# Kernel tuning notes

Measured on AMD Instinct MI355X. Metric: run time of the kernel, lower is better.

## Reference

```python
import jax, jax.numpy as jnp
import numpy as np

EMBED = 512
HEADS = 1
HEAD_DIM = EMBED // HEADS  # 512 (heads must be 1 for the original torch code to run)
N, S = 4, 4096


def setup_inputs() -> dict:
    key = jax.random.key(0)
    ks = jax.random.split(key, 9)
    scale = 1.0 / np.sqrt(EMBED)
    return {
        "values": jax.random.normal(ks[0], (N, 1, S, EMBED), dtype=jnp.float32),
        "keys": jax.random.normal(ks[1], (N, 1, S, EMBED), dtype=jnp.float32),
        "query": jax.random.normal(ks[2], (N, 1, S, EMBED), dtype=jnp.float32),
        "mask": jax.random.randint(ks[3], (N, 1, S, S), 0, 2, dtype=jnp.int32),
        "Wv": jax.random.normal(ks[4], (EMBED, EMBED), dtype=jnp.float32) * scale,
        "Wk": jax.random.normal(ks[5], (EMBED, EMBED), dtype=jnp.float32) * scale,
        "Wq": jax.random.normal(ks[6], (EMBED, EMBED), dtype=jnp.float32) * scale,
        "Wo": jax.random.normal(ks[7], (EMBED, EMBED), dtype=jnp.float32) * scale,
        "bo": jnp.zeros((EMBED,), dtype=jnp.float32),
    }


def reference(values, keys, query, mask, Wv, Wk, Wq, Wo, bo):
    n = query.shape[0]
    q_len = query.shape[2]
    # reshape(N, -1, heads, head_dim); inputs are [N, 1, S, E] -> [N, S, H, Dh]
    v = values.reshape(n, -1, HEADS, HEAD_DIM)
    k = keys.reshape(n, -1, HEADS, HEAD_DIM)
    q = query.reshape(n, -1, HEADS, HEAD_DIM)
    # per-module linear projections (nn.Linear: y = x @ W.T)
    v = jnp.einsum('nlhd,ed->nlhe', v, Wv)
    k = jnp.einsum('nlhd,ed->nlhe', k, Wk)
    q = jnp.einsum('nqhd,ed->nqhe', q, Wq)
    # full [N, H, Q, K] score matrix, as in the original
    energy = jnp.einsum('nqhd,nkhd->nhqk', q, k)
    energy = jnp.where(mask == 0, jnp.float32(-1e20), energy)
    attn = jax.nn.softmax(energy / np.sqrt(HEAD_DIM), axis=3)
    out = jnp.einsum('nhql,nlhd->nqhd', attn, v).reshape(n, q_len, HEADS * HEAD_DIM)
    return out @ Wo.T + bo
```

## Files before the change

### kernel.cpp

```cpp
#include <hip/hip_runtime.h>

typedef __bf16 bf16x8 __attribute__((ext_vector_type(8)));
typedef __bf16 bf16x4 __attribute__((ext_vector_type(4)));
typedef float f32x4 __attribute__((ext_vector_type(4)));
typedef float f32x16 __attribute__((ext_vector_type(16)));

#define MFMA16(a, b, c) __builtin_amdgcn_mfma_f32_16x16x32_bf16((a), (b), (c), 0, 0, 0)
#define MFMA32(a, b, c) __builtin_amdgcn_mfma_f32_32x32x16_bf16((a), (b), (c), 0, 0, 0)

static constexpr int SEQ = 4096;
static constexpr int DIM = 512;

typedef __attribute__((address_space(3))) void lds_void;
typedef __attribute__((address_space(1))) const void gbl_void;

__device__ __forceinline__ void glds16(const void* g, void* l) {
    __builtin_amdgcn_global_load_lds((gbl_void*)g, (lds_void*)l, 16, 0, 0);
}

__device__ __forceinline__ bf16x8 cvt8f(const float* __restrict__ p) {
    float4 f0 = *(const float4*)p;
    float4 f1 = *(const float4*)(p + 4);
    bf16x8 v;
    v[0] = (__bf16)f0.x; v[1] = (__bf16)f0.y; v[2] = (__bf16)f0.z; v[3] = (__bf16)f0.w;
    v[4] = (__bf16)f1.x; v[5] = (__bf16)f1.y; v[6] = (__bf16)f1.z; v[7] = (__bf16)f1.w;
    return v;
}

__global__ __launch_bounds__(256)
void cvt_f32_bf16(const float* __restrict__ in, __bf16* __restrict__ out) {
    const size_t i = ((size_t)blockIdx.x * 256 + threadIdx.x) * 8;
    *(bf16x8*)(out + i) = cvt8f(in + i);
}

__global__ __launch_bounds__(256)
void convert_w(const float* __restrict__ wq, const float* __restrict__ wk,
               const float* __restrict__ wv, const float* __restrict__ wo,
               __bf16* __restrict__ out)
{
    const int z = blockIdx.y;
    const float* src = (z == 0) ? wq : (z == 1) ? wk : (z == 2) ? wv : wo;
    __bf16* dst = out + (size_t)z * DIM * DIM;
    const int i = (blockIdx.x * 256 + threadIdx.x) * 8;
    *(bf16x8*)(dst + i) = cvt8f(src + i);
}

template <bool TRANS>
__global__ __launch_bounds__(256, 3)
void gemm_bf16(const __bf16* __restrict__ Ap, const __bf16* __restrict__ Bp,
               __bf16* __restrict__ Cp)
{
    __shared__ __align__(16) char smem[128 * 132 * 2];
    __bf16* As = (__bf16*)smem;
    __bf16* Bs = (__bf16*)(smem + 16384);

    const int tid  = threadIdx.x;
    const int wave = tid >> 6;
    const int lane = tid & 63;
    const int quad = lane >> 4;
    const int l16  = lane & 15;
    const int m0 = blockIdx.x * 128;
    const int n0 = blockIdx.y * 128;
    const int wm = (wave >> 1) * 64;
    const int wn = (wave & 1) * 64;

    f32x4 acc[4][4] = {};

    for (int k0 = 0; k0 < DIM; k0 += 64) {
        #pragma unroll
        for (int i = 0; i < 4; i++) {
            const int j = wave * 4 + i;
            const int c = j * 64 + lane;
            const int row = c >> 3, c8 = c & 7;
            glds16(Ap + (size_t)(m0 + row) * DIM + k0 + c8 * 8, &As[j * 512]);
            glds16(Bp + (size_t)(n0 + row) * DIM + k0 + c8 * 8, &Bs[j * 512]);
        }
        __syncthreads();
        #pragma unroll
        for (int kk = 0; kk < 2; kk++) {
            bf16x8 af[4], bg[4];
            #pragma unroll
            for (int mt = 0; mt < 4; mt++)
                af[mt] = *(const bf16x8*)&As[(wm + mt * 16 + l16) * 64 + kk * 32 + quad * 8];
            #pragma unroll
            for (int nt = 0; nt < 4; nt++)
                bg[nt] = *(const bf16x8*)&Bs[(wn + nt * 16 + l16) * 64 + kk * 32 + quad * 8];
            #pragma unroll
            for (int mt = 0; mt < 4; mt++)
                #pragma unroll
                for (int nt = 0; nt < 4; nt++)
                    acc[mt][nt] = MFMA16(af[mt], bg[nt], acc[mt][nt]);
        }
        __syncthreads();
    }

    if (!TRANS) {
        #pragma unroll
        for (int mt = 0; mt < 4; mt++)
            #pragma unroll
            for (int nt = 0; nt < 4; nt++)
                #pragma unroll
                for (int r = 0; r < 4; r++)
                    Cp[(size_t)(m0 + wm + mt * 16 + quad * 4 + r) * DIM
                       + n0 + wn + nt * 16 + l16] = (__bf16)acc[mt][nt][r];
    } else {
        __bf16* Tt = (__bf16*)smem;
        #pragma unroll
        for (int mt = 0; mt < 4; mt++)
            #pragma unroll
            for (int nt = 0; nt < 4; nt++)
                #pragma unroll
                for (int r = 0; r < 4; r++)
                    Tt[(wm + mt * 16 + quad * 4 + r) * 132 + wn + nt * 16 + l16]
                        = (__bf16)acc[mt][nt][r];
        __syncthreads();
        const int nb  = m0 >> 12;
        const int s0m = m0 & 4095;
        const int d   = tid >> 1;
        const int sh  = (tid & 1) * 64;
        __bf16* dst = Cp + (size_t)nb * DIM * SEQ + (size_t)(n0 + d) * SEQ + s0m + sh;
        #pragma unroll
        for (int i = 0; i < 8; i++) {
            bf16x8 vv;
            #pragma unroll
            for (int e = 0; e < 8; e++) vv[e] = Tt[(sh + i * 8 + e) * 132 + d];
            *(bf16x8*)(dst + i * 8) = vv;
        }
    }
}

__global__ __launch_bounds__(256, 3)
void gemm_out(const __bf16* __restrict__ Ap, const __bf16* __restrict__ Bp,
              float* __restrict__ Cp, const float* __restrict__ bias)
{
    __shared__ __align__(16) __bf16 As[128 * 64];
    __shared__ __align__(16) __bf16 Bs[128 * 64];
    const int tid  = threadIdx.x;
    const int wave = tid >> 6;
    const int lane = tid & 63;
    const int quad = lane >> 4;
    const int l16  = lane & 15;
    const int m0 = blockIdx.x * 128;
    const int n0 = blockIdx.y * 128;
    const int wm = (wave >> 1) * 64;
    const int wn = (wave & 1) * 64;

    f32x4 acc[4][4] = {};

    for (int k0 = 0; k0 < DIM; k0 += 64) {
        #pragma unroll
        for (int i = 0; i < 4; i++) {
            const int j = wave * 4 + i;
            const int c = j * 64 + lane;
            const int row = c >> 3, c8 = c & 7;
            glds16(Ap + (size_t)(m0 + row) * DIM + k0 + c8 * 8, &As[j * 512]);
            glds16(Bp + (size_t)(n0 + row) * DIM + k0 + c8 * 8, &Bs[j * 512]);
        }
        __syncthreads();
        #pragma unroll
        for (int kk = 0; kk < 2; kk++) {
            bf16x8 af[4], bg[4];
            #pragma unroll
            for (int mt = 0; mt < 4; mt++)
                af[mt] = *(const bf16x8*)&As[(wm + mt * 16 + l16) * 64 + kk * 32 + quad * 8];
            #pragma unroll
            for (int nt = 0; nt < 4; nt++)
                bg[nt] = *(const bf16x8*)&Bs[(wn + nt * 16 + l16) * 64 + kk * 32 + quad * 8];
            #pragma unroll
            for (int mt = 0; mt < 4; mt++)
                #pragma unroll
                for (int nt = 0; nt < 4; nt++)
                    acc[mt][nt] = MFMA16(af[mt], bg[nt], acc[mt][nt]);
        }
        __syncthreads();
    }
    #pragma unroll
    for (int mt = 0; mt < 4; mt++)
        #pragma unroll
        for (int nt = 0; nt < 4; nt++)
            #pragma unroll
            for (int r = 0; r < 4; r++) {
                const int col = n0 + wn + nt * 16 + l16;
                Cp[(size_t)(m0 + wm + mt * 16 + quad * 4 + r) * DIM + col]
                    = acc[mt][nt][r] + bias[col];
            }
}

__global__ __launch_bounds__(512, 2)
void flash_attn(__bf16* __restrict__ Qp, const __bf16* __restrict__ Kp,
                const __bf16* __restrict__ Vt, const int* __restrict__ mask)
{
    constexpr float SCALE = 0.044194173824159216f;

    __shared__ __bf16 Qs[64 * 512];
    __shared__ __bf16 KV[256 * 64];
    __shared__ __bf16 P[64 * 256];
    __shared__ unsigned Wb[8 * 66];
    __shared__ float pmax[8 * 66];
    __shared__ float psum[8 * 66];

    const int bid  = blockIdx.x;
    const int n    = bid & 3;
    const int q0   = (bid >> 2) * 64;
    const int tid  = threadIdx.x;
    const int w    = tid >> 6;
    const int lane = tid & 63;
    const int l32  = lane & 31;
    const int half = lane >> 5;
    const int r8   = lane >> 3;
    const int c8   = lane & 7;
    const int gc   = c8 ^ r8;

    const __bf16* Qb = Qp + (size_t)n * SEQ * DIM;
    const __bf16* Kb = Kp + (size_t)n * SEQ * DIM;
    const __bf16* Vb = Vt + (size_t)n * DIM * SEQ;
    const int*    Mb = mask + (size_t)n * SEQ * SEQ;
    __bf16*       AO = Qp + (size_t)n * SEQ * DIM;

    #pragma unroll
    for (int i = 0; i < 8; i++) {
        const int row = i * 8 + w;
        const int cs  = (lane & 56) | ((lane & 7) ^ (row & 7));
        glds16(Qb + (size_t)(q0 + row) * DIM + cs * 8, &Qs[row * 512]);
    }

    float m0 = -__builtin_inff(), m1 = -__builtin_inff();
    float l0 = 0.f, l1 = 0.f;
    f32x16 o00 = {}, o01 = {}, o10 = {}, o11 = {};

    const int mq = tid >> 3;
    const int wd = tid & 7;

    #pragma unroll 1
    for (int j = 0; j < 16; j++) {
        const int k0 = j * 256;

        int4 mk[8];
        {
            const int* mp = Mb + (size_t)(q0 + mq) * SEQ + k0 + wd * 32;
            #pragma unroll
            for (int c = 0; c < 8; c++) mk[c] = *(const int4*)(mp + c * 4);
        }

        f32x16 s0 = {}, s1 = {};
        #pragma unroll 1
        for (int dc = 0; dc < 8; dc++) {
            #pragma unroll
            for (int i = 0; i < 4; i++) {
                const int R = (i * 8 + w) * 8 + r8;
                glds16(Kb + (size_t)(k0 + R) * DIM + dc * 64 + gc * 8,
                       &KV[(i * 8 + w) * 512]);
            }
            __syncthreads();
            #pragma unroll
            for (int ks = 0; ks < 4; ks++) {
                const int row = 32 * w + l32;
                const int ca  = (2 * ks + half) ^ (row & 7);
                bf16x8 a = *(const bf16x8*)&KV[row * 64 + ca * 8];
                const int cq = dc * 8 + 2 * ks + half;
                const int pq = (cq & 56) | ((cq & 7) ^ (l32 & 7));
                bf16x8 b0 = *(const bf16x8*)&Qs[l32 * 512 + pq * 8];
                bf16x8 b1 = *(const bf16x8*)&Qs[(32 + l32) * 512 + pq * 8];
                s0 = MFMA32(a, b0, s0);
                s1 = MFMA32(a, b1, s1);
            }
            __syncthreads();
        }

        {
            unsigned wv = 0;
            #pragma unroll
            for (int c = 0; c < 8; c++) {
                wv |= (unsigned)(mk[c].x & 1) << (c * 4);
                wv |= (unsigned)(mk[c].y & 1) << (c * 4 + 1);
                wv |= (unsigned)(mk[c].z & 1) << (c * 4 + 2);
                wv |= (unsigned)(mk[c].w & 1) << (c * 4 + 3);
            }
            Wb[wd * 66 + mq] = wv;
        }
        {
            float mx0 = s0[0], mx1 = s1[0];
            #pragma unroll
            for (int r = 1; r < 16; r++) { mx0 = fmaxf(mx0, s0[r]); mx1 = fmaxf(mx1, s1[r]); }
            mx0 = fmaxf(mx0, __shfl_xor(mx0, 32));
            mx1 = fmaxf(mx1, __shfl_xor(mx1, 32));
            if (half == 0) pmax[w * 66 + l32]      = mx0;
            else           pmax[w * 66 + 32 + l32] = mx1;
        }
        __syncthreads();

        float mp0 = pmax[l32], mp1 = pmax[32 + l32];
        #pragma unroll
        for (int w2 = 1; w2 < 8; w2++) {
            mp0 = fmaxf(mp0, pmax[w2 * 66 + l32]);
            mp1 = fmaxf(mp1, pmax[w2 * 66 + 32 + l32]);
        }
        const float mn0 = fmaxf(m0, mp0 * SCALE);
        const float mn1 = fmaxf(m1, mp1 * SCALE);
        const float a0 = __expf(m0 - mn0);
        const float a1 = __expf(m1 - mn1);
        m0 = mn0; m1 = mn1;
        #pragma unroll
        for (int r = 0; r < 16; r++) {
            o00[r] *= a0; o10[r] *= a0;
            o01[r] *= a1; o11[r] *= a1;
        }

        float ls0 = 0.f, ls1 = 0.f;
        {
            const unsigned wm0 = Wb[w * 66 + l32];
            const unsigned wm1 = Wb[w * 66 + 32 + l32];
            #pragma unroll
            for (int g = 0; g < 4; g++) {
                bf16x4 pv0, pv1;
                #pragma unroll
                for (int r4 = 0; r4 < 4; r4++) {
                    const int r = g * 4 + r4;
                    const int bit = g * 8 + half * 4 + r4;
                    float p0 = __expf(s0[r] * SCALE - mn0);
                    float p1 = __expf(s1[r] * SCALE - mn1);
                    p0 = ((wm0 >> bit) & 1u) ? p0 : 0.f;
                    p1 = ((wm1 >> bit) & 1u) ? p1 : 0.f;
                    ls0 += p0; ls1 += p1;
                    pv0[r4] = (__bf16)p0;
                    pv1[r4] = (__bf16)p1;
                }
                const int c  = 4 * w + g;
                const int cp = (c & 24) | ((c & 7) ^ (l32 & 7));
                *(bf16x4*)&P[l32 * 256 + cp * 8 + 4 * half]        = pv0;
                *(bf16x4*)&P[(32 + l32) * 256 + cp * 8 + 4 * half] = pv1;
            }
            ls0 += __shfl_xor(ls0, 32);
            ls1 += __shfl_xor(ls1, 32);
            if (half == 0) psum[w * 66 + l32]      = ls0;
            else           psum[w * 66 + 32 + l32] = ls1;
        }
        __syncthreads();

        {
            float ss0 = 0.f, ss1 = 0.f;
            #pragma unroll
            for (int w2 = 0; w2 < 8; w2++) {
                ss0 += psum[w2 * 66 + l32];
                ss1 += psum[w2 * 66 + 32 + l32];
            }
            l0 = l0 * a0 + ss0;
            l1 = l1 * a1 + ss1;
        }

        #pragma unroll 1
        for (int h = 0; h < 2; h++) {
            #pragma unroll 1
            for (int kc2 = 0; kc2 < 4; kc2++) {
                #pragma unroll
                for (int i = 0; i < 4; i++) {
                    const int R = (i * 8 + w) * 8 + r8;
                    glds16(Vb + (size_t)(h * 256 + R) * SEQ + k0 + kc2 * 64 + gc * 8,
                           &KV[(i * 8 + w) * 512]);
                }
                __syncthreads();
                #pragma unroll
                for (int ks = 0; ks < 4; ks++) {
                    const int row = 32 * w + l32;
                    const int ca  = (2 * ks + half) ^ (row & 7);
                    bf16x8 a = *(const bf16x8*)&KV[row * 64 + ca * 8];
                    const int ck = kc2 * 8 + 2 * ks + half;
                    const int cp = (ck & 24) | ((ck & 7) ^ (l32 & 7));
                    bf16x8 b0 = *(const bf16x8*)&P[l32 * 256 + cp * 8];
                    bf16x8 b1 = *(const bf16x8*)&P[(32 + l32) * 256 + cp * 8];
                    if (h == 0) { o00 = MFMA32(a, b0, o00); o01 = MFMA32(a, b1, o01); }
                    else        { o10 = MFMA32(a, b0, o10); o11 = MFMA32(a, b1, o11); }
                }
                __syncthreads();
            }
        }
    }

    const float li0 = 1.f / l0, li1 = 1.f / l1;
    __bf16* ao0 = AO + (size_t)(q0 + l32) * DIM;
    __bf16* ao1 = AO + (size_t)(q0 + 32 + l32) * DIM;
    #pragma unroll
    for (int h = 0; h < 2; h++) {
        #pragma unroll
        for (int g = 0; g < 4; g++) {
            bf16x4 v00, v01;
            #pragma unroll
            for (int r4 = 0; r4 < 4; r4++) {
                const int r = g * 4 + r4;
                v00[r4] = (__bf16)((h ? o10[r] : o00[r]) * li0);
                v01[r4] = (__bf16)((h ? o11[r] : o01[r]) * li1);
            }
            const int d = h * 256 + 32 * w + g * 8 + 4 * half;
            *(bf16x4*)&ao0[d] = v00;
            *(bf16x4*)&ao1[d] = v01;
        }
    }
}

extern "C" void kernel_launch(void* const* d_in, const int* in_sizes, int n_in,
                              void* d_out, int out_size, void* d_ws, size_t ws_size,
                              hipStream_t stream)
{
    const float* values = (const float*)d_in[0];
    const float* keys   = (const float*)d_in[1];
    const float* query  = (const float*)d_in[2];
    const int*   mask   = (const int*)d_in[3];
    const float* Wv = (const float*)d_in[4];
    const float* Wk = (const float*)d_in[5];
    const float* Wq = (const float*)d_in[6];
    const float* Wo = (const float*)d_in[7];
    const float* bo = (const float*)d_in[8];
    float* out = (float*)d_out;

    char* ws = (char*)d_ws;
    __bf16* Qp  = (__bf16*)(ws);
    __bf16* Kp  = (__bf16*)(ws + (16u << 20));
    __bf16* Vt  = (__bf16*)(ws + (32u << 20));
    __bf16* Abf = (__bf16*)(ws + (48u << 20));
    __bf16* wbf = (__bf16*)(ws + (64u << 20));

    const int M = 4 * SEQ;
    const dim3 gg(M / 128, DIM / 128);

    convert_w<<<dim3(128, 4), 256, 0, stream>>>(Wq, Wk, Wv, Wo, wbf);

    cvt_f32_bf16<<<4096, 256, 0, stream>>>(query, Abf);
    gemm_bf16<false><<<gg, 256, 0, stream>>>(Abf, wbf + 0 * DIM * DIM, Qp);

    cvt_f32_bf16<<<4096, 256, 0, stream>>>(keys, Abf);
    gemm_bf16<false><<<gg, 256, 0, stream>>>(Abf, wbf + 1 * DIM * DIM, Kp);

    cvt_f32_bf16<<<4096, 256, 0, stream>>>(values, Abf);
    gemm_bf16<true><<<gg, 256, 0, stream>>>(Abf, wbf + 2 * DIM * DIM, Vt);

    flash_attn<<<256, 512, 0, stream>>>(Qp, Kp, Vt, mask);

    gemm_out<<<gg, 256, 0, stream>>>(Qp , wbf + 3 * DIM * DIM, out, bo);
}
```

Measured before the change: 808.9 us.

## Double-buffer K/V/Q staging in flash attention and load mask per-thread directly

Replaces the single K/V LDS buffer and resident full Q tile with a two-slot ring buffer. Each slot holds a K or V chunk plus the matching 64-column Q slice, and the next chunk is prefetched while MFMAs run on the current one, which halves the barriers per chunk. Mask values are loaded straight into the register layout of the score fragment, removing the bit-packed LDS mask exchange. MFMA phases are wrapped in s_setprio. Occupancy is lowered to one 512-thread block per CU and Q is reloaded from global memory for every key block.

```diff
diff --git a/kernel.cpp b/kernel.cpp
--- a/kernel.cpp
+++ b/kernel.cpp
@@ -186,16 +186,16 @@
             }
 }
 
-__global__ __launch_bounds__(512, 2)
+#define MKC(v, r4) ((r4) == 0 ? (v).x : (r4) == 1 ? (v).y : (r4) == 2 ? (v).z : (v).w)
+
+__global__ __launch_bounds__(512, 1)
 void flash_attn(__bf16* __restrict__ Qp, const __bf16* __restrict__ Kp,
                 const __bf16* __restrict__ Vt, const int* __restrict__ mask)
 {
     constexpr float SCALE = 0.044194173824159216f;
 
-    __shared__ __bf16 Qs[64 * 512];
-    __shared__ __bf16 KV[256 * 64];
+    __shared__ __bf16 KQ[2][20480];
     __shared__ __bf16 P[64 * 256];
-    __shared__ unsigned Wb[8 * 66];
     __shared__ float pmax[8 * 66];
     __shared__ float psum[8 * 66];
 
@@ -217,86 +217,92 @@
     const int*    Mb = mask + (size_t)n * SEQ * SEQ;
     __bf16*       AO = Qp + (size_t)n * SEQ * DIM;
 
-    #pragma unroll
-    for (int i = 0; i < 8; i++) {
-        const int row = i * 8 + w;
-        const int cs  = (lane & 56) | ((lane & 7) ^ (row & 7));
-        glds16(Qb + (size_t)(q0 + row) * DIM + cs * 8, &Qs[row * 512]);
-    }
+    auto stageK = [&](int slot, int k0, int dc) {
+        #pragma unroll
+        for (int i = 0; i < 4; i++) {
+            const int R = (i * 8 + w) * 8 + r8;
+            glds16(Kb + (size_t)(k0 + R) * DIM + dc * 64 + gc * 8,
+                   &KQ[slot][(i * 8 + w) * 512]);
+        }
+    };
+    auto stageV = [&](int slot, int k0, int vc) {
+        const int h = vc >> 2, kc2 = vc & 3;
+        #pragma unroll
+        for (int i = 0; i < 4; i++) {
+            const int R = (i * 8 + w) * 8 + r8;
+            glds16(Vb + (size_t)(h * 256 + R) * SEQ + k0 + kc2 * 64 + gc * 8,
+                   &KQ[slot][(i * 8 + w) * 512]);
+        }
+    };
+    auto stageQ = [&](int slot, int dc) {
+        glds16(Qb + (size_t)(q0 + w * 8 + r8) * DIM + dc * 64 + gc * 8,
+               &KQ[slot][16384 + w * 512]);
+    };
 
     float m0 = -__builtin_inff(), m1 = -__builtin_inff();
     float l0 = 0.f, l1 = 0.f;
     f32x16 o00 = {}, o01 = {}, o10 = {}, o11 = {};
 
-    const int mq = tid >> 3;
-    const int wd = tid & 7;
+    stageK(0, 0, 0);
+    stageQ(0, 0);
+    __syncthreads();
+    int cur = 0;
 
     #pragma unroll 1
     for (int j = 0; j < 16; j++) {
         const int k0 = j * 256;
 
-        int4 mk[8];
+        int4 mk0[4], mk1[4];
         {
-            const int* mp = Mb + (size_t)(q0 + mq) * SEQ + k0 + wd * 32;
-            #pragma unroll
-            for (int c = 0; c < 8; c++) mk[c] = *(const int4*)(mp + c * 4);
+            const int* mp0 = Mb + (size_t)(q0 + l32) * SEQ + k0 + 32 * w + 4 * half;
+            const int* mp1 = mp0 + (size_t)32 * SEQ;
+            #pragma unroll
+            for (int g = 0; g < 4; g++) {
+                mk0[g] = *(const int4*)(mp0 + 8 * g);
+                mk1[g] = *(const int4*)(mp1 + 8 * g);
+            }
         }
 
         f32x16 s0 = {}, s1 = {};
         #pragma unroll 1
         for (int dc = 0; dc < 8; dc++) {
-            #pragma unroll
-            for (int i = 0; i < 4; i++) {
-                const int R = (i * 8 + w) * 8 + r8;
-                glds16(Kb + (size_t)(k0 + R) * DIM + dc * 64 + gc * 8,
-                       &KV[(i * 8 + w) * 512]);
-            }
-            __syncthreads();
+            const int nxt = cur ^ 1;
+            if (dc < 7) { stageK(nxt, k0, dc + 1); stageQ(nxt, dc + 1); }
+            else        { stageV(nxt, k0, 0); }
+            const __bf16* Kc = KQ[cur];
+            const __bf16* Qc = KQ[cur] + 16384;
+            __builtin_amdgcn_s_setprio(1);
             #pragma unroll
             for (int ks = 0; ks < 4; ks++) {
-                const int row = 32 * w + l32;
-                const int ca  = (2 * ks + half) ^ (row & 7);
-                bf16x8 a = *(const bf16x8*)&KV[row * 64 + ca * 8];
-                const int cq = dc * 8 + 2 * ks + half;
-                const int pq = (cq & 56) | ((cq & 7) ^ (l32 & 7));
-                bf16x8 b0 = *(const bf16x8*)&Qs[l32 * 512 + pq * 8];
-                bf16x8 b1 = *(const bf16x8*)&Qs[(32 + l32) * 512 + pq * 8];
+                const int ch = (2 * ks + half) ^ (l32 & 7);
+                bf16x8 a  = *(const bf16x8*)&Kc[(32 * w + l32) * 64 + ch * 8];
+                bf16x8 b0 = *(const bf16x8*)&Qc[l32 * 64 + ch * 8];
+                bf16x8 b1 = *(const bf16x8*)&Qc[(32 + l32) * 64 + ch * 8];
                 s0 = MFMA32(a, b0, s0);
                 s1 = MFMA32(a, b1, s1);
             }
+            __builtin_amdgcn_s_setprio(0);
+            if (dc == 7) {
+                float mx0 = s0[0], mx1 = s1[0];
+                #pragma unroll
+                for (int r = 1; r < 16; r++) { mx0 = fmaxf(mx0, s0[r]); mx1 = fmaxf(mx1, s1[r]); }
+                mx0 = fmaxf(mx0, __shfl_xor(mx0, 32));
+                mx1 = fmaxf(mx1, __shfl_xor(mx1, 32));
+                if (half == 0) pmax[w * 66 + l32]      = mx0;
+                else           pmax[w * 66 + 32 + l32] = mx1;
+            }
             __syncthreads();
-        }
-
-        {
-            unsigned wv = 0;
-            #pragma unroll
-            for (int c = 0; c < 8; c++) {
-                wv |= (unsigned)(mk[c].x & 1) << (c * 4);
-                wv |= (unsigned)(mk[c].y & 1) << (c * 4 + 1);
-                wv |= (unsigned)(mk[c].z & 1) << (c * 4 + 2);
-                wv |= (unsigned)(mk[c].w & 1) << (c * 4 + 3);
-            }
-            Wb[wd * 66 + mq] = wv;
-        }
-        {
-            float mx0 = s0[0], mx1 = s1[0];
-            #pragma unroll
-            for (int r = 1; r < 16; r++) { mx0 = fmaxf(mx0, s0[r]); mx1 = fmaxf(mx1, s1[r]); }
-            mx0 = fmaxf(mx0, __shfl_xor(mx0, 32));
-            mx1 = fmaxf(mx1, __shfl_xor(mx1, 32));
-            if (half == 0) pmax[w * 66 + l32]      = mx0;
-            else           pmax[w * 66 + 32 + l32] = mx1;
-        }
-        __syncthreads();
-
-        float mp0 = pmax[l32], mp1 = pmax[32 + l32];
+            cur = nxt;
+        }
+
+        float mp0v = pmax[l32], mp1v = pmax[32 + l32];
         #pragma unroll
         for (int w2 = 1; w2 < 8; w2++) {
-            mp0 = fmaxf(mp0, pmax[w2 * 66 + l32]);
-            mp1 = fmaxf(mp1, pmax[w2 * 66 + 32 + l32]);
-        }
-        const float mn0 = fmaxf(m0, mp0 * SCALE);
-        const float mn1 = fmaxf(m1, mp1 * SCALE);
+            mp0v = fmaxf(mp0v, pmax[w2 * 66 + l32]);
+            mp1v = fmaxf(mp1v, pmax[w2 * 66 + 32 + l32]);
+        }
+        const float mn0 = fmaxf(m0, mp0v * SCALE);
+        const float mn1 = fmaxf(m1, mp1v * SCALE);
         const float a0 = __expf(m0 - mn0);
         const float a1 = __expf(m1 - mn1);
         m0 = mn0; m1 = mn1;
@@ -307,34 +313,29 @@
         }
 
         float ls0 = 0.f, ls1 = 0.f;
-        {
-            const unsigned wm0 = Wb[w * 66 + l32];
-            const unsigned wm1 = Wb[w * 66 + 32 + l32];
-            #pragma unroll
-            for (int g = 0; g < 4; g++) {
-                bf16x4 pv0, pv1;
-                #pragma unroll
-                for (int r4 = 0; r4 < 4; r4++) {
-                    const int r = g * 4 + r4;
-                    const int bit = g * 8 + half * 4 + r4;
-                    float p0 = __expf(s0[r] * SCALE - mn0);
-                    float p1 = __expf(s1[r] * SCALE - mn1);
-                    p0 = ((wm0 >> bit) & 1u) ? p0 : 0.f;
-                    p1 = ((wm1 >> bit) & 1u) ? p1 : 0.f;
-                    ls0 += p0; ls1 += p1;
-                    pv0[r4] = (__bf16)p0;
-                    pv1[r4] = (__bf16)p1;
-                }
-                const int c  = 4 * w + g;
-                const int cp = (c & 24) | ((c & 7) ^ (l32 & 7));
-                *(bf16x4*)&P[l32 * 256 + cp * 8 + 4 * half]        = pv0;
-                *(bf16x4*)&P[(32 + l32) * 256 + cp * 8 + 4 * half] = pv1;
-            }
-            ls0 += __shfl_xor(ls0, 32);
-            ls1 += __shfl_xor(ls1, 32);
-            if (half == 0) psum[w * 66 + l32]      = ls0;
-            else           psum[w * 66 + 32 + l32] = ls1;
-        }
+        #pragma unroll
+        for (int g = 0; g < 4; g++) {
+            bf16x4 pv0, pv1;
+            #pragma unroll
+            for (int r4 = 0; r4 < 4; r4++) {
+                const int r = g * 4 + r4;
+                float p0 = __expf(s0[r] * SCALE - mn0);
+                float p1 = __expf(s1[r] * SCALE - mn1);
+                p0 = MKC(mk0[g], r4) ? p0 : 0.f;
+                p1 = MKC(mk1[g], r4) ? p1 : 0.f;
+                ls0 += p0; ls1 += p1;
+                pv0[r4] = (__bf16)p0;
+                pv1[r4] = (__bf16)p1;
+            }
+            const int c  = 4 * w + g;
+            const int cp = (c & 24) | ((c & 7) ^ (l32 & 7));
+            *(bf16x4*)&P[l32 * 256 + cp * 8 + 4 * half]        = pv0;
+            *(bf16x4*)&P[(32 + l32) * 256 + cp * 8 + 4 * half] = pv1;
+        }
+        ls0 += __shfl_xor(ls0, 32);
+        ls1 += __shfl_xor(ls1, 32);
+        if (half == 0) psum[w * 66 + l32]      = ls0;
+        else           psum[w * 66 + 32 + l32] = ls1;
         __syncthreads();
 
         {
@@ -349,30 +350,27 @@
         }
 
         #pragma unroll 1
-        for (int h = 0; h < 2; h++) {
-            #pragma unroll 1
-            for (int kc2 = 0; kc2 < 4; kc2++) {
-                #pragma unroll
-                for (int i = 0; i < 4; i++) {
-                    const int R = (i * 8 + w) * 8 + r8;
-                    glds16(Vb + (size_t)(h * 256 + R) * SEQ + k0 + kc2 * 64 + gc * 8,
-                           &KV[(i * 8 + w) * 512]);
-                }
-                __syncthreads();
-                #pragma unroll
-                for (int ks = 0; ks < 4; ks++) {
-                    const int row = 32 * w + l32;
-                    const int ca  = (2 * ks + half) ^ (row & 7);
-                    bf16x8 a = *(const bf16x8*)&KV[row * 64 + ca * 8];
-                    const int ck = kc2 * 8 + 2 * ks + half;
-                    const int cp = (ck & 24) | ((ck & 7) ^ (l32 & 7));
-                    bf16x8 b0 = *(const bf16x8*)&P[l32 * 256 + cp * 8];
-                    bf16x8 b1 = *(const bf16x8*)&P[(32 + l32) * 256 + cp * 8];
-                    if (h == 0) { o00 = MFMA32(a, b0, o00); o01 = MFMA32(a, b1, o01); }
-                    else        { o10 = MFMA32(a, b0, o10); o11 = MFMA32(a, b1, o11); }
-                }
-                __syncthreads();
-            }
+        for (int vc = 0; vc < 8; vc++) {
+            const int nxt = cur ^ 1;
+            if (vc < 7)       stageV(nxt, k0, vc + 1);
+            else if (j < 15) { stageK(nxt, k0 + 256, 0); stageQ(nxt, 0); }
+            const __bf16* Vc = KQ[cur];
+            const int kc2 = vc & 3;
+            __builtin_amdgcn_s_setprio(1);
+            #pragma unroll
+            for (int ks = 0; ks < 4; ks++) {
+                const int ca = (2 * ks + half) ^ (l32 & 7);
+                bf16x8 a = *(const bf16x8*)&Vc[(32 * w + l32) * 64 + ca * 8];
+                const int ck = kc2 * 8 + 2 * ks + half;
+                const int cp = (ck & 24) | ((ck & 7) ^ (l32 & 7));
+                bf16x8 b0 = *(const bf16x8*)&P[l32 * 256 + cp * 8];
+                bf16x8 b1 = *(const bf16x8*)&P[(32 + l32) * 256 + cp * 8];
+                if (vc < 4) { o00 = MFMA32(a, b0, o00); o01 = MFMA32(a, b1, o01); }
+                else        { o10 = MFMA32(a, b0, o10); o11 = MFMA32(a, b1, o11); }
+            }
+            __builtin_amdgcn_s_setprio(0);
+            __syncthreads();
+            cur = nxt;
         }
     }
 
```

Measured after the change: 734.8 us. -9.2%, faster.
